# Performance work log

Hardware: AMD Instinct MI355X
Metric: run time of the kernel (lower is better)

## Reference

```python
import jax, jax.numpy as jnp
import numpy as np
from jax import lax

LAMBDA = 0.1
THETA = 1.0
BETA = 1.0
MAX_ITER = 100

SOBEL_X = jnp.array([[-1., 0., 1.], [-2., 0., 2.], [-1., 0., 1.]], dtype=jnp.float32)
SOBEL_Y = jnp.array([[-1., -2., -1.], [0., 0., 0.], [1., 2., 1.]], dtype=jnp.float32)
DIV_X = jnp.array([[0., 0., 0.], [-1., 0., 1.], [0., 0., 0.]], dtype=jnp.float32)
DIV_Y = jnp.array([[0., -1., 0.], [0., 0., 0.], [0., 1., 0.]], dtype=jnp.float32)


def _conv(x, k):
    # x: [B,1,H,W], k: [3,3]; torch conv2d is cross-correlation, same as lax default
    return lax.conv_general_dilated(x, k[None, None], (1, 1), 'SAME',
                                    dimension_numbers=('NCHW', 'OIHW', 'NCHW'))


def setup_inputs() -> dict:
    key = jax.random.key(0)
    f = jax.random.uniform(key, (4, 1, 512, 512), dtype=jnp.float32)
    return {"f": f}


def _forward(f):
    gx = _conv(f, SOBEL_X)
    gy = _conv(f, SOBEL_Y)
    g = 1.0 / (1.0 + BETA * (gx ** 2 + gy ** 2))  # beta * grad_mag**2
    thr = THETA * LAMBDA

    def body(carry, _):
        p1, p2, u, v = carry
        div_p = _conv(p1, DIV_X) + _conv(p2, DIV_Y)
        r = div_p - (f - v) / THETA
        rgx = _conv(r, SOBEL_X / 8.0)
        rgy = _conv(r, SOBEL_Y / 8.0)
        denom = 1.0 + 0.125 * jnp.sqrt(rgx ** 2 + rgy ** 2) / g
        p1 = (p1 + 0.125 * rgx) / denom
        p2 = (p2 + 0.125 * rgy) / denom
        div_p = _conv(p1, DIV_X) + _conv(p2, DIV_Y)
        u = f - v - THETA * div_p
        diff = f - u
        v = jnp.where(diff > thr, diff - thr,
                      jnp.where(diff < -thr, diff + thr, jnp.zeros_like(diff)))
        return (p1, p2, u, v), None

    z = jnp.zeros_like(f)
    (p1, p2, u, v), _ = lax.scan(body, (z, z, f, z), None, length=MAX_ITER)
    return u


def reference(f):
    return _forward(f)
```

## Files before the change

### kernel.cpp

```cpp
#include <hip/hip_runtime.h>

#define IMH 512
#define IMW 512
#define NB 4
#define NPIX (IMH*IMW)

#define TX 64
#define TY 32
#define GXT 8
#define GYT 16
#define NBLK (GXT*GYT*NB)
#define NTH 1024

#define PW2 88
#define P_H2 50
#define VW2 80
#define V_H2 48

#define PIDX(y,x) (((y)+9)*PW2 + ((x)+12))
#define VIDX(y,x) (((y)+8)*VW2 + ((x)+8))

__device__ __forceinline__ float4 lds4(const float* p, int i){ return *(const float4*)(p + i); }
__device__ __forceinline__ void  sts4(float* p, int i, float4 v){ *(float4*)(p + i) = v; }
__device__ __forceinline__ float4 f4zero(){ return make_float4(0.f,0.f,0.f,0.f); }
__device__ __forceinline__ float shrink01(float d){
  return d - fminf(fmaxf(d, -0.1f), 0.1f);
}

template<bool EDGE>
__device__ __forceinline__ float4 gld4(const float* base, int gy, int gx){
  if (EDGE){ gy = min(max(gy,0),IMH-1); gx = min(max(gx,0),IMW-4); }
  return *(const float4*)(base + gy*IMW + gx);
}
__device__ __forceinline__ float4 mask4(float4 v, int gy, int gx){
  if ((unsigned)gy >= (unsigned)IMH) return f4zero();
  v.x = ((unsigned)(gx+0) < (unsigned)IMW) ? v.x : 0.f;
  v.y = ((unsigned)(gx+1) < (unsigned)IMW) ? v.y : 0.f;
  v.z = ((unsigned)(gx+2) < (unsigned)IMW) ? v.z : 0.f;
  v.w = ((unsigned)(gx+3) < (unsigned)IMW) ? v.w : 0.f;
  return v;
}

struct RowS { float lw; float4 m; float rx; };
__device__ __forceinline__ RowS load_rowS(const float* A, int base, int lo, int ro){
  RowS q; q.m = lds4(A, base); q.lw = A[base+lo]; q.rx = A[base+ro]; return q;
}
__device__ __forceinline__ float4 dxvS(const RowS& q){
  return make_float4(q.m.y - q.lw, q.m.z - q.m.x, q.m.w - q.m.y, q.rx - q.m.z);
}
__device__ __forceinline__ void sobel_rowsS(const RowS& A, const RowS& B, const RowS& C,
                                            float4& rgx, float4& rgy){
  float4 da = dxvS(A), db = dxvS(B), dc = dxvS(C);
  rgx.x = (da.x + 2.f*db.x + dc.x) * 0.125f;
  rgx.y = (da.y + 2.f*db.y + dc.y) * 0.125f;
  rgx.z = (da.z + 2.f*db.z + dc.z) * 0.125f;
  rgx.w = (da.w + 2.f*db.w + dc.w) * 0.125f;
  float cm1 = C.lw - A.lw;
  float c0 = C.m.x - A.m.x, c1 = C.m.y - A.m.y;
  float c2 = C.m.z - A.m.z, c3 = C.m.w - A.m.w;
  float c4 = C.rx - A.rx;
  rgy.x = (cm1 + 2.f*c0 + c1) * 0.125f;
  rgy.y = (c0  + 2.f*c1 + c2) * 0.125f;
  rgy.z = (c1  + 2.f*c2 + c3) * 0.125f;
  rgy.w = (c2  + 2.f*c3 + c4) * 0.125f;
}
__device__ __forceinline__ void p_elem(float4 rgx, float4 rgy, float4 pa, float4 pb,
                                       float4 gg, float4& n1, float4& n2){
#define PE(c) { \
    float mag = __builtin_amdgcn_sqrtf(rgx.c*rgx.c + rgy.c*rgy.c); \
    float inv = __builtin_amdgcn_rcpf(1.f + 0.125f*mag*gg.c); \
    n1.c = (pa.c + 0.125f*rgx.c)*inv; n2.c = (pb.c + 0.125f*rgy.c)*inv; }
  PE(x) PE(y) PE(z) PE(w)
#undef PE
}

template<bool EDGE>
__device__ __forceinline__ void p_phase(const float* Rs, float* P1s, float* P2s,
    const float* gb, int x0, int y0, int tid, int ylo, int nrows){
  int total = nrows * 20;
  for (int i = tid; i < total; i += NTH){
    int cy = i / 20, cx = i - cy*20;
    int x = cx*4 - 8;
    int y = ylo + cy;
    int col = x + 8;
    int lo = (col==0) ? 0 : -1;
    int ro = (col==76) ? 0 : 4;
    int base = VIDX(y,x);
    RowS Rm1 = load_rowS(Rs, base-VW2, lo, ro);
    RowS R0  = load_rowS(Rs, base,     lo, ro);
    RowS R1  = load_rowS(Rs, base+VW2, lo, ro);
    float4 rgx, rgy;
    sobel_rowsS(Rm1, R0, R1, rgx, rgy);
    int p0 = PIDX(y,x);
    float4 pa = lds4(P1s,p0), pb = lds4(P2s,p0);
    float4 g0 = gld4<EDGE>(gb, y0+y, x0+x);
    float4 n1, n2;
    p_elem(rgx,rgy,pa,pb,g0,n1,n2);
    if (EDGE){
      n1 = mask4(n1, y0+y, x0+x); n2 = mask4(n2, y0+y, x0+x);
    }
    sts4(P1s,p0,n1); sts4(P2s,p0,n2);
  }
}

template<bool EDGE, bool FIRSTR>
__device__ __forceinline__ void vr_phase(float* Rs, const float* P1s, const float* P2s,
    float4& vreg, const float* fb, int x0, int y0, int vy, int vx, bool vown,
    int ylo, int nrows){
  if (!vown) return;
  if (vy < ylo || vy >= ylo + nrows) return;
  int y = vy, x = vx;
  int pc = PIDX(y,x);
  float4 m = lds4(P1s,pc);
  float lw = P1s[pc-1], rx = P1s[pc+4];
  float4 up = lds4(P2s,pc-PW2), dn = lds4(P2s,pc+PW2);
  float4 db;
  db.x = (m.y - lw)  + (dn.x - up.x);
  db.y = (m.z - m.x) + (dn.y - up.y);
  db.z = (m.w - m.y) + (dn.z - up.z);
  db.w = (rx  - m.z) + (dn.w - up.w);
  float4 ff = gld4<EDGE>(fb, y0+y, x0+x);
  float4 rv;
  if (!FIRSTR){
    vreg.x = shrink01(vreg.x + db.x); vreg.y = shrink01(vreg.y + db.y);
    vreg.z = shrink01(vreg.z + db.z); vreg.w = shrink01(vreg.w + db.w);
  }
  rv.x = db.x - ff.x + vreg.x; rv.y = db.y - ff.y + vreg.y;
  rv.z = db.z - ff.z + vreg.z; rv.w = db.w - ff.w + vreg.w;
  if (EDGE) rv = mask4(rv, y0+y, x0+x);
  sts4(Rs, VIDX(y,x), rv);
}

template<bool FIRST, bool LAST, bool EDGE>
__device__ __forceinline__ void iter_body4(
    const float* fb, const float* gb,
    const float* p1b, const float* p2b, const float* vb,
    float* p1o, float* p2o, float* vo, float* uo,
    int x0, int y0, int tid,
    float* P1s, float* P2s, float* Rs)
{
  const bool vown = tid < 960;
  const int vcy = tid / 20, vcx = tid - vcy*20;
  const int vy = vcy - 8, vx = vcx*4 - 8;

  for (int i = tid; i < 50*22; i += NTH){
    int cy = i / 22, cx = i - cy*22;
    int x = cx*4 - 12, y = cy - 9;
    float4 a, b;
    if (FIRST){ a = f4zero(); b = f4zero(); }
    else {
      int gy = y0+y, gx = x0+x;
      a = gld4<EDGE>(p1b, gy, gx); b = gld4<EDGE>(p2b, gy, gx);
      if (EDGE){ a = mask4(a,gy,gx); b = mask4(b,gy,gx); }
    }
    int idx = PIDX(y,x);
    sts4(P1s, idx, a); sts4(P2s, idx, b);
  }
  float4 vreg = f4zero();
  if (!FIRST && vown){
    int gy = y0+vy, gx = x0+vx;
    vreg = gld4<EDGE>(vb, gy, gx);
    if (EDGE) vreg = mask4(vreg, gy, gx);
  }
  __syncthreads();

  vr_phase<EDGE,true >(Rs,P1s,P2s,vreg,fb,x0,y0,vy,vx,vown,-8,48); __syncthreads();
  p_phase<EDGE>(Rs,P1s,P2s,gb,x0,y0,tid,-7,46);                    __syncthreads();
  vr_phase<EDGE,false>(Rs,P1s,P2s,vreg,fb,x0,y0,vy,vx,vown,-6,44); __syncthreads();
  p_phase<EDGE>(Rs,P1s,P2s,gb,x0,y0,tid,-5,42);                    __syncthreads();
  vr_phase<EDGE,false>(Rs,P1s,P2s,vreg,fb,x0,y0,vy,vx,vown,-4,40); __syncthreads();
  p_phase<EDGE>(Rs,P1s,P2s,gb,x0,y0,tid,-3,38);                    __syncthreads();
  vr_phase<EDGE,false>(Rs,P1s,P2s,vreg,fb,x0,y0,vy,vx,vown,-2,36); __syncthreads();
  p_phase<EDGE>(Rs,P1s,P2s,gb,x0,y0,tid,-1,34);                    __syncthreads();

  if (vown && vy >= 0 && vy < TY && vx >= 0 && vx < TX){
    int y = vy, x = vx;
    int pc = PIDX(y,x);
    float4 m = lds4(P1s,pc);
    float lw = P1s[pc-1], rx = P1s[pc+4];
    float4 up = lds4(P2s,pc-PW2), dn = lds4(P2s,pc+PW2);
    float4 dq;
    dq.x = (m.y - lw)  + (dn.x - up.x);
    dq.y = (m.z - m.x) + (dn.y - up.y);
    dq.z = (m.w - m.y) + (dn.z - up.z);
    dq.w = (rx  - m.z) + (dn.w - up.w);
    size_t go = (size_t)(y0+y)*IMW + (x0+x);
    if (LAST){
      float4 ff = gld4<false>(fb, y0+y, x0+x);
      float4 uu;
      uu.x = ff.x - vreg.x - dq.x; uu.y = ff.y - vreg.y - dq.y;
      uu.z = ff.z - vreg.z - dq.z; uu.w = ff.w - vreg.w - dq.w;
      *(float4*)(uo + go) = uu;
    } else {
      float4 m2 = lds4(P2s,pc);
      float4 vn;
      vn.x = shrink01(vreg.x + dq.x); vn.y = shrink01(vreg.y + dq.y);
      vn.z = shrink01(vreg.z + dq.z); vn.w = shrink01(vreg.w + dq.w);
      *(float4*)(p1o + go) = m;
      *(float4*)(p2o + go) = m2;
      *(float4*)(vo  + go) = vn;
    }
  }
}

template<bool FIRST, bool LAST>
__global__ __launch_bounds__(NTH, 8) void iter4_kernel(
    const float* __restrict__ f, const float* __restrict__ ginv,
    const float* __restrict__ p1in, const float* __restrict__ p2in,
    const float* __restrict__ vin,
    float* __restrict__ p1out, float* __restrict__ p2out,
    float* __restrict__ vout, float* __restrict__ uout)
{
  __shared__ alignas(16) float P1s[P_H2*PW2], P2s[P_H2*PW2];
  __shared__ alignas(16) float Rs[V_H2*VW2];

  int phys = blockIdx.x;
  int virt = (phys & 7) * (NBLK/8) + (phys >> 3);
  int bx = virt & (GXT-1);
  int by = (virt >> 3) & (GYT-1);
  int b  = virt >> 7;
  int x0 = bx*TX, y0 = by*TY;
  size_t boff = (size_t)b * NPIX;
  bool edge = (bx==0) | (bx==GXT-1) | (by==0) | (by==GYT-1);
  int tid = threadIdx.x;

  if (edge)
    iter_body4<FIRST,LAST,true>(f+boff, ginv+boff, p1in+boff, p2in+boff, vin+boff,
        p1out+boff, p2out+boff, vout+boff, uout+boff, x0, y0, tid,
        P1s, P2s, Rs);
  else
    iter_body4<FIRST,LAST,false>(f+boff, ginv+boff, p1in+boff, p2in+boff, vin+boff,
        p1out+boff, p2out+boff, vout+boff, uout+boff, x0, y0, tid,
        P1s, P2s, Rs);
}

__global__ __launch_bounds__(256) void init_kernel(
    const float* __restrict__ f, float* __restrict__ ginv) {
  int i = blockIdx.x * 256 + threadIdx.x;
  int b = i >> 16; int rem = i & 0xFFFF;
  int gy = rem >> 7; int gx = (rem & 127) * 4;
  const float* fb = f + (size_t)b * NPIX;
  float L[3], R[3]; float4 O[3];
  for (int k = 0; k < 3; ++k){
    int y = gy + k - 1;
    if ((unsigned)y < (unsigned)IMH){
      const float* rp = fb + (size_t)y*IMW + gx;
      O[k] = *(const float4*)rp;
      L[k] = (gx > 0) ? rp[-1] : 0.f;
      R[k] = (gx < IMW-4) ? rp[4] : 0.f;
    } else { O[k] = f4zero(); L[k] = 0.f; R[k] = 0.f; }
  }
  float4 out;
#define GE(c, im1, i0, ip1) { \
    float sx = (i0##_p - i0##_m)*2.f + (im1##_p - im1##_m) + (ip1##_p - ip1##_m); \
    float sy = (ip1##_m - im1##_m) + 2.f*(ip1##_c - im1##_c) + (ip1##_p - im1##_p); \
    out.c = 1.f + sx*sx + sy*sy; }
  { float a_m=L[0], a_c=O[0].x, a_p=O[0].y;
    float b_m=L[1], b_c=O[1].x, b_p=O[1].y;
    float c_m=L[2], c_c=O[2].x, c_p=O[2].y;
    GE(x, a, b, c) }
  { float a_m=O[0].x, a_c=O[0].y, a_p=O[0].z;
    float b_m=O[1].x, b_c=O[1].y, b_p=O[1].z;
    float c_m=O[2].x, c_c=O[2].y, c_p=O[2].z;
    GE(y, a, b, c) }
  { float a_m=O[0].y, a_c=O[0].z, a_p=O[0].w;
    float b_m=O[1].y, b_c=O[1].z, b_p=O[1].w;
    float c_m=O[2].y, c_c=O[2].z, c_p=O[2].w;
    GE(z, a, b, c) }
  { float a_m=O[0].z, a_c=O[0].w, a_p=R[0];
    float b_m=O[1].z, b_c=O[1].w, b_p=R[1];
    float c_m=O[2].z, c_c=O[2].w, c_p=R[2];
    GE(w, a, b, c) }
#undef GE
  *(float4*)(ginv + (size_t)b*NPIX + (size_t)gy*IMW + gx) = out;
}

extern "C" void kernel_launch(void* const* d_in, const int* in_sizes, int n_in,
                              void* d_out, int out_size, void* d_ws, size_t ws_size,
                              hipStream_t stream) {
  const float* f = (const float*)d_in[0];
  float* u = (float*)d_out;
  float* ws = (float*)d_ws;
  const size_t N = (size_t)NB * NPIX;
  float* g   = ws + 0*N;
  float* p1a = ws + 1*N;
  float* p2a = ws + 2*N;
  float* va  = ws + 3*N;
  float* p1b = ws + 4*N;
  float* p2b = ws + 5*N;
  float* vb  = ws + 6*N;

  init_kernel<<<1024, 256, 0, stream>>>(f, g);

  for (int l = 0; l < 25; ++l) {
    const float *pi1, *pi2, *vi;
    float *po1, *po2, *vo;
    if (l & 1) { pi1 = p1b; pi2 = p2b; vi = vb; po1 = p1a; po2 = p2a; vo = va; }
    else       { pi1 = p1a; pi2 = p2a; vi = va; po1 = p1b; po2 = p2b; vo = vb; }
    if (l == 0)
      iter4_kernel<true, false><<<NBLK, NTH, 0, stream>>>(f, g, pi1, pi2, vi, po1, po2, vo, u);
    else if (l == 24)
      iter4_kernel<false, true><<<NBLK, NTH, 0, stream>>>(f, g, pi1, pi2, vi, po1, po2, vo, u);
    else
      iter4_kernel<false, false><<<NBLK, NTH, 0, stream>>>(f, g, pi1, pi2, vi, po1, po2, vo, u);
  }
}
```

Baseline: 394.9 us.

## Fuse five iterations per launch with wider halo temporal tiling

```diff
diff --git a/kernel.cpp b/kernel.cpp
--- a/kernel.cpp
+++ b/kernel.cpp
@@ -13,12 +13,12 @@
 #define NTH 1024
 
 #define PW2 88
-#define P_H2 50
-#define VW2 80
-#define V_H2 48
-
-#define PIDX(y,x) (((y)+9)*PW2 + ((x)+12))
-#define VIDX(y,x) (((y)+8)*VW2 + ((x)+8))
+#define P_H2 54
+#define VW2 88
+#define V_H2 52
+
+#define PIDX(y,x) (((y)+11)*PW2 + ((x)+12))
+#define VIDX(y,x) (((y)+10)*VW2 + ((x)+12))
 
 __device__ __forceinline__ float4 lds4(const float* p, int i){ return *(const float4*)(p + i); }
 __device__ __forceinline__ void  sts4(float* p, int i, float4 v){ *(float4*)(p + i) = v; }
@@ -74,17 +74,50 @@
 #undef PE
 }
 
-template<bool EDGE>
+__device__ __forceinline__ float4 divp_at(const float* P1s, const float* P2s, int pc){
+  float4 m = lds4(P1s,pc);
+  float lw = P1s[pc-1], rx = P1s[pc+4];
+  float4 up = lds4(P2s,pc-PW2), dn = lds4(P2s,pc+PW2);
+  float4 db;
+  db.x = (m.y - lw)  + (dn.x - up.x);
+  db.y = (m.z - m.x) + (dn.y - up.y);
+  db.z = (m.w - m.y) + (dn.z - up.z);
+  db.w = (rx  - m.z) + (dn.w - up.w);
+  return db;
+}
+
+template<bool FIRST, bool EDGE>
+__device__ __forceinline__ void vr1_phase(float* Rs, const float* P1s, const float* P2s,
+    const float* vb, const float* fb, int x0, int y0, int tid){
+  for (int i = tid; i < 52*22; i += NTH){
+    int cy = i / 22, cx = i - cy*22;
+    int x = cx*4 - 12, y = cy - 10;
+    float4 db = divp_at(P1s, P2s, PIDX(y,x));
+    float4 ff = gld4<EDGE>(fb, y0+y, x0+x);
+    float4 vv = f4zero();
+    if (!FIRST){
+      vv = gld4<EDGE>(vb, y0+y, x0+x);
+      if (EDGE) vv = mask4(vv, y0+y, x0+x);
+    }
+    float4 rv;
+    rv.x = db.x - ff.x + vv.x; rv.y = db.y - ff.y + vv.y;
+    rv.z = db.z - ff.z + vv.z; rv.w = db.w - ff.w + vv.w;
+    if (EDGE) rv = mask4(rv, y0+y, x0+x);
+    sts4(Rs, VIDX(y,x), rv);
+  }
+}
+
+template<bool EDGE, int CPR, int XBASE>
 __device__ __forceinline__ void p_phase(const float* Rs, float* P1s, float* P2s,
     const float* gb, int x0, int y0, int tid, int ylo, int nrows){
-  int total = nrows * 20;
+  int total = nrows * CPR;
   for (int i = tid; i < total; i += NTH){
-    int cy = i / 20, cx = i - cy*20;
-    int x = cx*4 - 8;
+    int cy = i / CPR, cx = i - cy*CPR;
+    int x = cx*4 + XBASE;
     int y = ylo + cy;
-    int col = x + 8;
+    int col = x + 12;
     int lo = (col==0) ? 0 : -1;
-    int ro = (col==76) ? 0 : 4;
+    int ro = (col==84) ? 0 : 4;
     int base = VIDX(y,x);
     RowS Rm1 = load_rowS(Rs, base-VW2, lo, ro);
     RowS R0  = load_rowS(Rs, base,     lo, ro);
@@ -103,28 +136,18 @@
   }
 }
 
-template<bool EDGE, bool FIRSTR>
+template<bool EDGE>
 __device__ __forceinline__ void vr_phase(float* Rs, const float* P1s, const float* P2s,
     float4& vreg, const float* fb, int x0, int y0, int vy, int vx, bool vown,
     int ylo, int nrows){
   if (!vown) return;
   if (vy < ylo || vy >= ylo + nrows) return;
   int y = vy, x = vx;
-  int pc = PIDX(y,x);
-  float4 m = lds4(P1s,pc);
-  float lw = P1s[pc-1], rx = P1s[pc+4];
-  float4 up = lds4(P2s,pc-PW2), dn = lds4(P2s,pc+PW2);
-  float4 db;
-  db.x = (m.y - lw)  + (dn.x - up.x);
-  db.y = (m.z - m.x) + (dn.y - up.y);
-  db.z = (m.w - m.y) + (dn.z - up.z);
-  db.w = (rx  - m.z) + (dn.w - up.w);
+  float4 db = divp_at(P1s, P2s, PIDX(y,x));
   float4 ff = gld4<EDGE>(fb, y0+y, x0+x);
+  vreg.x = shrink01(vreg.x + db.x); vreg.y = shrink01(vreg.y + db.y);
+  vreg.z = shrink01(vreg.z + db.z); vreg.w = shrink01(vreg.w + db.w);
   float4 rv;
-  if (!FIRSTR){
-    vreg.x = shrink01(vreg.x + db.x); vreg.y = shrink01(vreg.y + db.y);
-    vreg.z = shrink01(vreg.z + db.z); vreg.w = shrink01(vreg.w + db.w);
-  }
   rv.x = db.x - ff.x + vreg.x; rv.y = db.y - ff.y + vreg.y;
   rv.z = db.z - ff.z + vreg.z; rv.w = db.w - ff.w + vreg.w;
   if (EDGE) rv = mask4(rv, y0+y, x0+x);
@@ -132,7 +155,7 @@
 }
 
 template<bool FIRST, bool LAST, bool EDGE>
-__device__ __forceinline__ void iter_body4(
+__device__ __forceinline__ void iter_body5(
     const float* fb, const float* gb,
     const float* p1b, const float* p2b, const float* vb,
     float* p1o, float* p2o, float* vo, float* uo,
@@ -143,9 +166,9 @@
   const int vcy = tid / 20, vcx = tid - vcy*20;
   const int vy = vcy - 8, vx = vcx*4 - 8;
 
-  for (int i = tid; i < 50*22; i += NTH){
+  for (int i = tid; i < 54*22; i += NTH){
     int cy = i / 22, cx = i - cy*22;
-    int x = cx*4 - 12, y = cy - 9;
+    int x = cx*4 - 12, y = cy - 11;
     float4 a, b;
     if (FIRST){ a = f4zero(); b = f4zero(); }
     else {
@@ -164,26 +187,21 @@
   }
   __syncthreads();
 
-  vr_phase<EDGE,true >(Rs,P1s,P2s,vreg,fb,x0,y0,vy,vx,vown,-8,48); __syncthreads();
-  p_phase<EDGE>(Rs,P1s,P2s,gb,x0,y0,tid,-7,46);                    __syncthreads();
-  vr_phase<EDGE,false>(Rs,P1s,P2s,vreg,fb,x0,y0,vy,vx,vown,-6,44); __syncthreads();
-  p_phase<EDGE>(Rs,P1s,P2s,gb,x0,y0,tid,-5,42);                    __syncthreads();
-  vr_phase<EDGE,false>(Rs,P1s,P2s,vreg,fb,x0,y0,vy,vx,vown,-4,40); __syncthreads();
-  p_phase<EDGE>(Rs,P1s,P2s,gb,x0,y0,tid,-3,38);                    __syncthreads();
-  vr_phase<EDGE,false>(Rs,P1s,P2s,vreg,fb,x0,y0,vy,vx,vown,-2,36); __syncthreads();
-  p_phase<EDGE>(Rs,P1s,P2s,gb,x0,y0,tid,-1,34);                    __syncthreads();
+  vr1_phase<FIRST,EDGE>(Rs,P1s,P2s,vb,fb,x0,y0,tid);                __syncthreads();
+  p_phase<EDGE,22,-12>(Rs,P1s,P2s,gb,x0,y0,tid,-9,50);              __syncthreads();
+  vr_phase<EDGE>(Rs,P1s,P2s,vreg,fb,x0,y0,vy,vx,vown,-8,48);        __syncthreads();
+  p_phase<EDGE,20,-8>(Rs,P1s,P2s,gb,x0,y0,tid,-7,46);               __syncthreads();
+  vr_phase<EDGE>(Rs,P1s,P2s,vreg,fb,x0,y0,vy,vx,vown,-6,44);        __syncthreads();
+  p_phase<EDGE,20,-8>(Rs,P1s,P2s,gb,x0,y0,tid,-5,42);               __syncthreads();
+  vr_phase<EDGE>(Rs,P1s,P2s,vreg,fb,x0,y0,vy,vx,vown,-4,40);        __syncthreads();
+  p_phase<EDGE,20,-8>(Rs,P1s,P2s,gb,x0,y0,tid,-3,38);               __syncthreads();
+  vr_phase<EDGE>(Rs,P1s,P2s,vreg,fb,x0,y0,vy,vx,vown,-2,36);        __syncthreads();
+  p_phase<EDGE,20,-8>(Rs,P1s,P2s,gb,x0,y0,tid,-1,34);               __syncthreads();
 
   if (vown && vy >= 0 && vy < TY && vx >= 0 && vx < TX){
     int y = vy, x = vx;
     int pc = PIDX(y,x);
-    float4 m = lds4(P1s,pc);
-    float lw = P1s[pc-1], rx = P1s[pc+4];
-    float4 up = lds4(P2s,pc-PW2), dn = lds4(P2s,pc+PW2);
-    float4 dq;
-    dq.x = (m.y - lw)  + (dn.x - up.x);
-    dq.y = (m.z - m.x) + (dn.y - up.y);
-    dq.z = (m.w - m.y) + (dn.z - up.z);
-    dq.w = (rx  - m.z) + (dn.w - up.w);
+    float4 dq = divp_at(P1s, P2s, pc);
     size_t go = (size_t)(y0+y)*IMW + (x0+x);
     if (LAST){
       float4 ff = gld4<false>(fb, y0+y, x0+x);
@@ -192,6 +210,7 @@
       uu.z = ff.z - vreg.z - dq.z; uu.w = ff.w - vreg.w - dq.w;
       *(float4*)(uo + go) = uu;
     } else {
+      float4 m  = lds4(P1s,pc);
       float4 m2 = lds4(P2s,pc);
       float4 vn;
       vn.x = shrink01(vreg.x + dq.x); vn.y = shrink01(vreg.y + dq.y);
@@ -204,7 +223,7 @@
 }
 
 template<bool FIRST, bool LAST>
-__global__ __launch_bounds__(NTH, 8) void iter4_kernel(
+__global__ __launch_bounds__(NTH, 8) void iter5_kernel(
     const float* __restrict__ f, const float* __restrict__ ginv,
     const float* __restrict__ p1in, const float* __restrict__ p2in,
     const float* __restrict__ vin,
@@ -225,11 +244,11 @@
   int tid = threadIdx.x;
 
   if (edge)
-    iter_body4<FIRST,LAST,true>(f+boff, ginv+boff, p1in+boff, p2in+boff, vin+boff,
+    iter_body5<FIRST,LAST,true>(f+boff, ginv+boff, p1in+boff, p2in+boff, vin+boff,
         p1out+boff, p2out+boff, vout+boff, uout+boff, x0, y0, tid,
         P1s, P2s, Rs);
   else
-    iter_body4<FIRST,LAST,false>(f+boff, ginv+boff, p1in+boff, p2in+boff, vin+boff,
+    iter_body5<FIRST,LAST,false>(f+boff, ginv+boff, p1in+boff, p2in+boff, vin+boff,
         p1out+boff, p2out+boff, vout+boff, uout+boff, x0, y0, tid,
         P1s, P2s, Rs);
 }
@@ -292,16 +311,16 @@
 
   init_kernel<<<1024, 256, 0, stream>>>(f, g);
 
-  for (int l = 0; l < 25; ++l) {
+  for (int l = 0; l < 20; ++l) {
     const float *pi1, *pi2, *vi;
     float *po1, *po2, *vo;
     if (l & 1) { pi1 = p1b; pi2 = p2b; vi = vb; po1 = p1a; po2 = p2a; vo = va; }
     else       { pi1 = p1a; pi2 = p2a; vi = va; po1 = p1b; po2 = p2b; vo = vb; }
     if (l == 0)
-      iter4_kernel<true, false><<<NBLK, NTH, 0, stream>>>(f, g, pi1, pi2, vi, po1, po2, vo, u);
-    else if (l == 24)
-      iter4_kernel<false, true><<<NBLK, NTH, 0, stream>>>(f, g, pi1, pi2, vi, po1, po2, vo, u);
+      iter5_kernel<true, false><<<NBLK, NTH, 0, stream>>>(f, g, pi1, pi2, vi, po1, po2, vo, u);
+    else if (l == 19)
+      iter5_kernel<false, true><<<NBLK, NTH, 0, stream>>>(f, g, pi1, pi2, vi, po1, po2, vo, u);
     else
-      iter4_kernel<false, false><<<NBLK, NTH, 0, stream>>>(f, g, pi1, pi2, vi, po1, po2, vo, u);
-  }
-}
+      iter5_kernel<false, false><<<NBLK, NTH, 0, stream>>>(f, g, pi1, pi2, vi, po1, po2, vo, u);
+  }
+}
```

Result: no change. 394.0 us (-0.2%).
